# Kernel tuning notes

Hardware: AMD Instinct MI355X
Metric: run time of the kernel (lower is better)

The kernel has to match this reference:

```python
import jax, jax.numpy as jnp
import numpy as np

N_NODES = 100000
N_EDGES = 1600000
IN_FEAT = 128
HIDDEN = 64
N_CLASSES = 16


def setup_inputs() -> dict:
    key = jax.random.key(0)
    ks = jax.random.split(key, 8)
    x = jax.random.normal(ks[0], (N_NODES, IN_FEAT), dtype=jnp.float32)
    edge_index = jax.random.randint(ks[1], (2, N_EDGES), 0, N_NODES, dtype=jnp.int64)
    W1 = jax.random.normal(ks[2], (IN_FEAT, HIDDEN), dtype=jnp.float32) / np.sqrt(IN_FEAT)
    b1 = jnp.zeros((HIDDEN,), dtype=jnp.float32)
    W2 = jax.random.normal(ks[3], (HIDDEN, HIDDEN), dtype=jnp.float32) / np.sqrt(HIDDEN)
    b2 = jnp.zeros((HIDDEN,), dtype=jnp.float32)
    Wl = jax.random.normal(ks[4], (HIDDEN, N_CLASSES), dtype=jnp.float32) / np.sqrt(HIDDEN)
    bl = jnp.zeros((N_CLASSES,), dtype=jnp.float32)
    return {"x": x, "edge_index": edge_index, "W1": W1, "b1": b1,
            "W2": W2, "b2": b2, "Wl": Wl, "bl": bl}


def _gcn_norm(edge_index, n_nodes, dtype):
    # PyG GCNConv default: add self-loops, symmetric normalization
    # A_hat = D^{-1/2} (A + I) D^{-1/2}, degree computed at destination (col).
    loop = jnp.arange(n_nodes, dtype=edge_index.dtype)
    src = jnp.concatenate([edge_index[0], loop])
    dst = jnp.concatenate([edge_index[1], loop])
    deg = jax.ops.segment_sum(jnp.ones_like(dst, dtype=dtype), dst, num_segments=n_nodes)
    dinv = jnp.where(deg > 0, jax.lax.rsqrt(deg), 0.0).astype(dtype)
    norm = dinv[src] * dinv[dst]  # [E + N]
    return src, dst, norm


def _gcn_conv(h, src, dst, norm, W, b, n_nodes):
    hw = h @ W                                  # [N, out] linear first (GCNConv order)
    msg = hw[src] * norm[:, None]               # gather + edge-normalize, [E+N, out]
    out = jax.ops.segment_sum(msg, dst, num_segments=n_nodes)  # scatter-add
    return out + b


def reference(x, edge_index, W1, b1, W2, b2, Wl, bl):
    n = x.shape[0]
    src, dst, norm = _gcn_norm(edge_index, n, x.dtype)
    h = jax.nn.relu(_gcn_conv(x, src, dst, norm, W1, b1, n))
    h = jax.nn.relu(_gcn_conv(h, src, dst, norm, W2, b2, n))
    return h @ Wl + bl  # [N, num_classes] logits
```

## Files before the change

kernel.cpp:

```cpp
#include <hip/hip_runtime.h>
#include <hip/hip_fp16.h>
#include <math.h>

#define N_NODES 100000
#define N_EDGES 1600000
#define IN_FEAT 128
#define HIDDEN 64
#define N_CLASSES 16

#define TM 64
#define GBLK ((N_NODES + TM - 1) / TM)

#define NBUK 196
#define CB 4096
#define NCB ((N_EDGES + CB - 1) / CB)
#define NHB 128


__global__ void zero_buk_k(int* __restrict__ buk_cnt) {
    if (threadIdx.x < NBUK + 4) buk_cnt[threadIdx.x] = 0;
}

__global__ __launch_bounds__(256) void bukhist_k(const int* __restrict__ dst,
                                                 int* __restrict__ buk_cnt) {
    __shared__ int hist[NBUK + 4];
    int tid = threadIdx.x;
    if (tid < NBUK) hist[tid] = 0;
    __syncthreads();
    const int n4 = N_EDGES >> 2;
    for (int i4 = blockIdx.x * 256 + tid; i4 < n4; i4 += NHB * 256) {
        int4 d4 = ((const int4*)dst)[i4];
        atomicAdd(&hist[d4.x >> 9], 1);
        atomicAdd(&hist[d4.y >> 9], 1);
        atomicAdd(&hist[d4.z >> 9], 1);
        atomicAdd(&hist[d4.w >> 9], 1);
    }
    __syncthreads();
    if (tid < NBUK && hist[tid] != 0) atomicAdd(&buk_cnt[tid], hist[tid]);
}

__global__ __launch_bounds__(256) void buk_scan_k(const int* __restrict__ buk_cnt,
                                                  int* __restrict__ buk_off,
                                                  int* __restrict__ bcur) {
    __shared__ int sm[256];
    int t = threadIdx.x;
    int v = (t < NBUK) ? buk_cnt[t] : 0;
    sm[t] = v;
    __syncthreads();
    for (int s = 1; s < 256; s <<= 1) {
        int add = (t >= s) ? sm[t - s] : 0;
        __syncthreads();
        sm[t] += add;
        __syncthreads();
    }
    if (t < NBUK) {
        int excl = sm[t] - v;
        buk_off[t] = excl;
        bcur[t] = excl;
    }
    if (t == 0) buk_off[NBUK] = N_EDGES;
}


__global__ __launch_bounds__(256) void coarse_k(const int* __restrict__ src,
                                                const int* __restrict__ dst,
                                                int* __restrict__ bcur,
                                                int2* __restrict__ pairs) {
    __shared__ int hist[NBUK + 4], loff[NBUK + 4], cur[NBUK + 4], gbase[NBUK + 4];
    __shared__ int sc[256];
    __shared__ int2 stage[CB];
    int tid = threadIdx.x;
    int eb = blockIdx.x * CB;
    int nvalid = N_EDGES - eb;
    if (nvalid > CB) nvalid = CB;

    if (tid < NBUK) hist[tid] = 0;
    __syncthreads();

    int4 s4[4], d4[4];
    #pragma unroll
    for (int q = 0; q < 4; ++q) {
        int e4 = (eb >> 2) + tid + q * 256;
        if (e4 * 4 < N_EDGES) {
            s4[q] = ((const int4*)src)[e4];
            d4[q] = ((const int4*)dst)[e4];
        } else {
            d4[q] = make_int4(-1, -1, -1, -1);
            s4[q] = make_int4(0, 0, 0, 0);
        }
    }
    #pragma unroll
    for (int q = 0; q < 4; ++q) {
        if (d4[q].x >= 0) {
            atomicAdd(&hist[d4[q].x >> 9], 1);
            atomicAdd(&hist[d4[q].y >> 9], 1);
            atomicAdd(&hist[d4[q].z >> 9], 1);
            atomicAdd(&hist[d4[q].w >> 9], 1);
        }
    }
    __syncthreads();

    int v = (tid < NBUK) ? hist[tid] : 0;
    sc[tid] = v;
    __syncthreads();
    for (int s = 1; s < 256; s <<= 1) {
        int add = (tid >= s) ? sc[tid - s] : 0;
        __syncthreads();
        sc[tid] += add;
        __syncthreads();
    }
    if (tid < NBUK) {
        int excl = sc[tid] - v;
        loff[tid] = excl;
        cur[tid] = excl;
        gbase[tid] = atomicAdd(&bcur[tid], v);
    }
    __syncthreads();

    #pragma unroll
    for (int q = 0; q < 4; ++q) {
        if (d4[q].x >= 0) {
            int b, r;
            b = d4[q].x >> 9; r = atomicAdd(&cur[b], 1); stage[r] = make_int2(s4[q].x, d4[q].x);
            b = d4[q].y >> 9; r = atomicAdd(&cur[b], 1); stage[r] = make_int2(s4[q].y, d4[q].y);
            b = d4[q].z >> 9; r = atomicAdd(&cur[b], 1); stage[r] = make_int2(s4[q].z, d4[q].z);
            b = d4[q].w >> 9; r = atomicAdd(&cur[b], 1); stage[r] = make_int2(s4[q].w, d4[q].w);
        }
    }
    __syncthreads();

    for (int i = tid; i < nvalid; i += 256) {
        int2 p = stage[i];
        int b = p.y >> 9;
        pairs[gbase[b] + (i - loff[b])] = p;
    }
}


__global__ __launch_bounds__(256) void fine2_k(const int2* __restrict__ pairs,
                                               const int* __restrict__ buk_off,
                                               int* __restrict__ csr_src,
                                               int* __restrict__ row_ptr,
                                               float* __restrict__ dinv) {
    __shared__ int cnt[512];
    __shared__ int psc[256];
    __shared__ int cur[512];
    int b = blockIdx.x;
    int node0 = b * 512;
    int nn = N_NODES - node0;
    if (nn > 512) nn = 512;
    int tid = threadIdx.x;

    cnt[tid] = 0; cnt[tid + 256] = 0;
    __syncthreads();

    int e0 = buk_off[b];
    int e1 = buk_off[b + 1];

    for (int e = e0 + tid; e < e1; e += 256)
        atomicAdd(&cnt[pairs[e].y - node0], 1);
    __syncthreads();

    int c0 = cnt[2 * tid], c1 = cnt[2 * tid + 1];
    int p = c0 + c1;
    psc[tid] = p;
    __syncthreads();
    for (int s = 1; s < 256; s <<= 1) {
        int add = (tid >= s) ? psc[tid - s] : 0;
        __syncthreads();
        psc[tid] += add;
        __syncthreads();
    }
    int excl = psc[tid] - p;
    int g0 = e0 + excl;
    int g1 = g0 + c0;
    cur[2 * tid] = g0;
    cur[2 * tid + 1] = g1;
    if (2 * tid < nn) {
        row_ptr[node0 + 2 * tid] = g0;
        dinv[node0 + 2 * tid] = 1.0f / sqrtf((float)(c0 + 1));
    }
    if (2 * tid + 1 < nn) {
        row_ptr[node0 + 2 * tid + 1] = g1;
        dinv[node0 + 2 * tid + 1] = 1.0f / sqrtf((float)(c1 + 1));
    }
    if (b == NBUK - 1 && tid == 0) row_ptr[N_NODES] = N_EDGES;
    __syncthreads();

    for (int e = e0 + tid; e < e1; e += 256) {
        int2 pr = pairs[e];
        int pos = atomicAdd(&cur[pr.y - node0], 1);
        csr_src[pos] = pr.x;
    }
}


__global__ __launch_bounds__(256) void gemm1_tiled_k(const float* __restrict__ x,
                                                     const float* __restrict__ W,
                                                     const float* __restrict__ dinv,
                                                     __half* __restrict__ hws_h) {
    __shared__ float Ws[64][64];
    __shared__ float xt[64][68];
    int tid = threadIdx.x;
    int row0 = blockIdx.x * TM;
    int rgrp4 = (tid >> 4) * 4;
    int cgrp4 = (tid & 15) * 4;

    float acc[4][4];
    #pragma unroll
    for (int r = 0; r < 4; ++r)
        #pragma unroll
        for (int c = 0; c < 4; ++c) acc[r][c] = 0.0f;

    for (int k0 = 0; k0 < IN_FEAT; k0 += 64) {
        #pragma unroll
        for (int i = 0; i < 4; ++i) {
            int f4 = tid + i * 256;
            int kk = f4 >> 4, c4 = (f4 & 15) * 4;
            *(float4*)&Ws[kk][c4] = *(const float4*)&W[(size_t)(k0 + kk) * HIDDEN + c4];
        }
        #pragma unroll
        for (int i = 0; i < 4; ++i) {
            int f4 = tid + i * 256;
            int rr = f4 >> 4, kq = (f4 & 15) * 4;
            int row = row0 + rr;
            if (row >= N_NODES) row = N_NODES - 1;
            float4 v = *(const float4*)&x[(size_t)row * IN_FEAT + k0 + kq];
            xt[kq + 0][rr] = v.x; xt[kq + 1][rr] = v.y;
            xt[kq + 2][rr] = v.z; xt[kq + 3][rr] = v.w;
        }
        __syncthreads();

        #pragma unroll 16
        for (int kk = 0; kk < 64; ++kk) {
            float4 a = *(const float4*)&xt[kk][rgrp4];
            float4 b = *(const float4*)&Ws[kk][cgrp4];
            acc[0][0] += a.x * b.x; acc[0][1] += a.x * b.y; acc[0][2] += a.x * b.z; acc[0][3] += a.x * b.w;
            acc[1][0] += a.y * b.x; acc[1][1] += a.y * b.y; acc[1][2] += a.y * b.z; acc[1][3] += a.y * b.w;
            acc[2][0] += a.z * b.x; acc[2][1] += a.z * b.y; acc[2][2] += a.z * b.z; acc[2][3] += a.z * b.w;
            acc[3][0] += a.w * b.x; acc[3][1] += a.w * b.y; acc[3][2] += a.w * b.z; acc[3][3] += a.w * b.w;
        }
        __syncthreads();
    }

    #pragma unroll
    for (int r = 0; r < 4; ++r) {
        int row = row0 + rgrp4 + r;
        if (row < N_NODES) {
            float dn = dinv[row];
            __half2* ph = (__half2*)&hws_h[(size_t)row * HIDDEN + cgrp4];
            ph[0] = __floats2half2_rn(acc[r][0] * dn, acc[r][1] * dn);
            ph[1] = __floats2half2_rn(acc[r][2] * dn, acc[r][3] * dn);
        }
    }
}


__global__ __launch_bounds__(256) void gemm2_tiled_k(const float* __restrict__ agg,
                                                     const float* __restrict__ W,
                                                     const float* __restrict__ dinv,
                                                     __half* __restrict__ hws_h) {
    __shared__ float Ws[64][64];
    __shared__ float xt[64][68];
    int tid = threadIdx.x;
    int row0 = blockIdx.x * TM;
    int rgrp4 = (tid >> 4) * 4;
    int cgrp4 = (tid & 15) * 4;

    #pragma unroll
    for (int i = 0; i < 4; ++i) {
        int f4 = tid + i * 256;
        int kk = f4 >> 4, c4 = (f4 & 15) * 4;
        *(float4*)&Ws[kk][c4] = *(const float4*)&W[(size_t)kk * HIDDEN + c4];
    }
    #pragma unroll
    for (int i = 0; i < 4; ++i) {
        int f4 = tid + i * 256;
        int rr = f4 >> 4, kq = (f4 & 15) * 4;
        int row = row0 + rr;
        if (row >= N_NODES) row = N_NODES - 1;
        float4 v = *(const float4*)&agg[(size_t)row * HIDDEN + kq];
        xt[kq + 0][rr] = fmaxf(v.x, 0.f); xt[kq + 1][rr] = fmaxf(v.y, 0.f);
        xt[kq + 2][rr] = fmaxf(v.z, 0.f); xt[kq + 3][rr] = fmaxf(v.w, 0.f);
    }
    __syncthreads();

    float acc[4][4];
    #pragma unroll
    for (int r = 0; r < 4; ++r)
        #pragma unroll
        for (int c = 0; c < 4; ++c) acc[r][c] = 0.0f;

    #pragma unroll 16
    for (int kk = 0; kk < 64; ++kk) {
        float4 a = *(const float4*)&xt[kk][rgrp4];
        float4 b = *(const float4*)&Ws[kk][cgrp4];
        acc[0][0] += a.x * b.x; acc[0][1] += a.x * b.y; acc[0][2] += a.x * b.z; acc[0][3] += a.x * b.w;
        acc[1][0] += a.y * b.x; acc[1][1] += a.y * b.y; acc[1][2] += a.y * b.z; acc[1][3] += a.y * b.w;
        acc[2][0] += a.z * b.x; acc[2][1] += a.z * b.y; acc[2][2] += a.z * b.z; acc[2][3] += a.z * b.w;
        acc[3][0] += a.w * b.x; acc[3][1] += a.w * b.y; acc[3][2] += a.w * b.z; acc[3][3] += a.w * b.w;
    }

    #pragma unroll
    for (int r = 0; r < 4; ++r) {
        int row = row0 + rgrp4 + r;
        if (row < N_NODES) {
            float dn = dinv[row];
            __half2* ph = (__half2*)&hws_h[(size_t)row * HIDDEN + cgrp4];
            ph[0] = __floats2half2_rn(acc[r][0] * dn, acc[r][1] * dn);
            ph[1] = __floats2half2_rn(acc[r][2] * dn, acc[r][3] * dn);
        }
    }
}


__global__ __launch_bounds__(256) void pull_k(const int* __restrict__ row_ptr,
                                              const int* __restrict__ csr_src,
                                              const float* __restrict__ dinv,
                                              const __half* __restrict__ hws_h,
                                              const float* __restrict__ b,
                                              float* __restrict__ agg) {
    int node = __builtin_amdgcn_readfirstlane((blockIdx.x * 256 + threadIdx.x) >> 6);
    int lane = threadIdx.x & 63;
    if (node >= N_NODES) return;

    int start = __builtin_amdgcn_readfirstlane(row_ptr[node]);
    int end   = __builtin_amdgcn_readfirstlane(row_ptr[node + 1]);

    const __half* __restrict__ selfrow = hws_h + ((size_t)node << 6);
    float blane = b[lane];
    float a0 = __half2float(selfrow[lane]);
    float dn = dinv[node];

    float a1 = 0.f, a2 = 0.f, a3 = 0.f, a4 = 0.f, a5 = 0.f, a6 = 0.f, a7 = 0.f;

    int base = start;
    while (base < end) {
        int rem = end - base;
        int ci = base + lane;
        int lastci = end - 1;
        if (ci > lastci) ci = lastci;
        int idxv = csr_src[ci];
        int nch = rem < 64 ? rem : 64;

        for (int j = 0; j < nch; j += 16) {
            #pragma unroll
            for (int k = 0; k < 16; ++k) {
                int jj = j + k;
                int s = __builtin_amdgcn_readlane(idxv, jj);
                const __half* __restrict__ row = hws_h + ((size_t)s << 6);
                float w = (jj < rem) ? 1.f : 0.f;
                float v = __half2float(row[lane]);
                if (k == 0)      a0 += w * v;
                else if (k == 1) a1 += w * v;
                else if (k == 2) a2 += w * v;
                else if (k == 3) a3 += w * v;
                else if (k == 4) a4 += w * v;
                else if (k == 5) a5 += w * v;
                else if (k == 6) a6 += w * v;
                else if (k == 7) a7 += w * v;
                else if (k == 8)  a0 += w * v;
                else if (k == 9)  a1 += w * v;
                else if (k == 10) a2 += w * v;
                else if (k == 11) a3 += w * v;
                else if (k == 12) a4 += w * v;
                else if (k == 13) a5 += w * v;
                else if (k == 14) a6 += w * v;
                else              a7 += w * v;
            }
        }
        base += 64;
    }

    float sum = ((a0 + a1) + (a2 + a3)) + ((a4 + a5) + (a6 + a7));
    float* __restrict__ outrow = agg + ((size_t)node << 6);
    outrow[lane] = blane + dn * sum;
}


__global__ __launch_bounds__(256) void final_k(const float* __restrict__ agg,
                                               const float* __restrict__ Wl,
                                               const float* __restrict__ bl,
                                               float* __restrict__ out) {
    __shared__ float Ws[HIDDEN * N_CLASSES];
    __shared__ float hs[16][HIDDEN + 1];
    int tid = threadIdx.x;

    if (tid < HIDDEN * N_CLASSES / 4) ((float4*)Ws)[tid] = ((const float4*)Wl)[tid];

    int row0 = blockIdx.x * 16;
    for (int i = tid; i < 16 * HIDDEN; i += 256) {
        int rr = i >> 6;
        int kk = i & 63;
        hs[rr][kk] = fmaxf(agg[(size_t)(row0 + rr) * HIDDEN + kk], 0.0f);
    }
    __syncthreads();

    int col = tid & 15;
    int r = tid >> 4;
    float acc = bl[col];
    #pragma unroll
    for (int k = 0; k < HIDDEN; ++k)
        acc += hs[r][k] * Ws[k * N_CLASSES + col];
    out[(size_t)(row0 + r) * N_CLASSES + col] = acc;
}


extern "C" void kernel_launch(void* const* d_in, const int* in_sizes, int n_in,
                              void* d_out, int out_size, void* d_ws, size_t ws_size,
                              hipStream_t stream) {
    const float* x  = (const float*)d_in[0];
    const int*   ei = (const int*)d_in[1];
    const float* W1 = (const float*)d_in[2];
    const float* b1 = (const float*)d_in[3];
    const float* W2 = (const float*)d_in[4];
    const float* b2 = (const float*)d_in[5];
    const float* Wl = (const float*)d_in[6];
    const float* bl = (const float*)d_in[7];
    float* out = (float*)d_out;

    const int* src = ei;
    const int* dst = ei + N_EDGES;

    __half* hws_h  = (__half*)d_ws;
    float* agg     = (float*)(hws_h + (size_t)N_NODES * HIDDEN);
    int2*  pairs   = (int2*)agg;
    int*   csr_src = (int*)(agg + (size_t)N_NODES * HIDDEN);
    float* dinv    = (float*)(csr_src + N_EDGES);
    int*   row_ptr = (int*)(dinv + N_NODES);
    int*   buk_cnt = row_ptr + N_NODES + 4;
    int*   buk_off = buk_cnt + 200;
    int*   bcur    = buk_off + 200;

    zero_buk_k<<<1, 256, 0, stream>>>(buk_cnt);
    bukhist_k<<<NHB, 256, 0, stream>>>(dst, buk_cnt);
    buk_scan_k<<<1, 256, 0, stream>>>(buk_cnt, buk_off, bcur);
    coarse_k<<<NCB, 256, 0, stream>>>(src, dst, bcur, pairs);
    fine2_k<<<NBUK, 256, 0, stream>>>(pairs, buk_off, csr_src, row_ptr, dinv);

    gemm1_tiled_k<<<GBLK, 256, 0, stream>>>(x, W1, dinv, hws_h);
    pull_k<<<(N_NODES * 64 + 255) / 256, 256, 0, stream>>>(row_ptr, csr_src, dinv,
                                                           hws_h, b1, agg);

    gemm2_tiled_k<<<GBLK, 256, 0, stream>>>(agg, W2, dinv, hws_h);
    pull_k<<<(N_NODES * 64 + 255) / 256, 256, 0, stream>>>(row_ptr, csr_src, dinv,
                                                           hws_h, b2, agg);

    final_k<<<N_NODES / 16, 256, 0, stream>>>(agg, Wl, bl, out);
}
```

Measured before the change: 289.7 us.

## Replace coarse bucket sort with per-block count/scan/place and restructure pull gather

```diff
diff --git a/kernel.cpp b/kernel.cpp
--- a/kernel.cpp
+++ b/kernel.cpp
@@ -14,125 +14,88 @@
 #define NBUK 196
 #define CB 4096
 #define NCB ((N_EDGES + CB - 1) / CB)
-#define NHB 128
-
-
-__global__ void zero_buk_k(int* __restrict__ buk_cnt) {
-    if (threadIdx.x < NBUK + 4) buk_cnt[threadIdx.x] = 0;
-}
-
-__global__ __launch_bounds__(256) void bukhist_k(const int* __restrict__ dst,
-                                                 int* __restrict__ buk_cnt) {
+
+
+__global__ __launch_bounds__(256) void count_k(const int* __restrict__ dst,
+                                               int* __restrict__ blk_cnt) {
     __shared__ int hist[NBUK + 4];
     int tid = threadIdx.x;
     if (tid < NBUK) hist[tid] = 0;
     __syncthreads();
-    const int n4 = N_EDGES >> 2;
-    for (int i4 = blockIdx.x * 256 + tid; i4 < n4; i4 += NHB * 256) {
-        int4 d4 = ((const int4*)dst)[i4];
-        atomicAdd(&hist[d4.x >> 9], 1);
-        atomicAdd(&hist[d4.y >> 9], 1);
-        atomicAdd(&hist[d4.z >> 9], 1);
-        atomicAdd(&hist[d4.w >> 9], 1);
-    }
-    __syncthreads();
-    if (tid < NBUK && hist[tid] != 0) atomicAdd(&buk_cnt[tid], hist[tid]);
-}
-
-__global__ __launch_bounds__(256) void buk_scan_k(const int* __restrict__ buk_cnt,
-                                                  int* __restrict__ buk_off,
-                                                  int* __restrict__ bcur) {
-    __shared__ int sm[256];
-    int t = threadIdx.x;
-    int v = (t < NBUK) ? buk_cnt[t] : 0;
-    sm[t] = v;
-    __syncthreads();
-    for (int s = 1; s < 256; s <<= 1) {
-        int add = (t >= s) ? sm[t - s] : 0;
-        __syncthreads();
-        sm[t] += add;
-        __syncthreads();
-    }
-    if (t < NBUK) {
-        int excl = sm[t] - v;
-        buk_off[t] = excl;
-        bcur[t] = excl;
-    }
-    if (t == 0) buk_off[NBUK] = N_EDGES;
-}
-
-
-__global__ __launch_bounds__(256) void coarse_k(const int* __restrict__ src,
-                                                const int* __restrict__ dst,
-                                                int* __restrict__ bcur,
-                                                int2* __restrict__ pairs) {
-    __shared__ int hist[NBUK + 4], loff[NBUK + 4], cur[NBUK + 4], gbase[NBUK + 4];
-    __shared__ int sc[256];
-    __shared__ int2 stage[CB];
-    int tid = threadIdx.x;
     int eb = blockIdx.x * CB;
-    int nvalid = N_EDGES - eb;
-    if (nvalid > CB) nvalid = CB;
-
-    if (tid < NBUK) hist[tid] = 0;
-    __syncthreads();
-
-    int4 s4[4], d4[4];
     #pragma unroll
     for (int q = 0; q < 4; ++q) {
         int e4 = (eb >> 2) + tid + q * 256;
         if (e4 * 4 < N_EDGES) {
-            s4[q] = ((const int4*)src)[e4];
-            d4[q] = ((const int4*)dst)[e4];
-        } else {
-            d4[q] = make_int4(-1, -1, -1, -1);
-            s4[q] = make_int4(0, 0, 0, 0);
-        }
-    }
+            int4 d4 = ((const int4*)dst)[e4];
+            atomicAdd(&hist[d4.x >> 9], 1);
+            atomicAdd(&hist[d4.y >> 9], 1);
+            atomicAdd(&hist[d4.z >> 9], 1);
+            atomicAdd(&hist[d4.w >> 9], 1);
+        }
+    }
+    __syncthreads();
+    if (tid < NBUK) blk_cnt[blockIdx.x * NBUK + tid] = hist[tid];
+}
+
+__global__ __launch_bounds__(512) void colscan_k(int* __restrict__ blk_cnt,
+                                                 int* __restrict__ coltot) {
+    __shared__ int sm[512];
+    int b = blockIdx.x;
+    int t = threadIdx.x;
+    int v = (t < NCB) ? blk_cnt[t * NBUK + b] : 0;
+    sm[t] = v;
+    __syncthreads();
+    for (int s = 1; s < 512; s <<= 1) {
+        int add = (t >= s) ? sm[t - s] : 0;
+        __syncthreads();
+        sm[t] += add;
+        __syncthreads();
+    }
+    if (t < NCB) blk_cnt[t * NBUK + b] = sm[t] - v;
+    if (t == NCB - 1) coltot[b] = sm[t];
+}
+
+__global__ __launch_bounds__(256) void bukoff_k(const int* __restrict__ coltot,
+                                                int* __restrict__ buk_off) {
+    __shared__ int sm[256];
+    int t = threadIdx.x;
+    int v = (t < NBUK) ? coltot[t] : 0;
+    sm[t] = v;
+    __syncthreads();
+    for (int s = 1; s < 256; s <<= 1) {
+        int add = (t >= s) ? sm[t - s] : 0;
+        __syncthreads();
+        sm[t] += add;
+        __syncthreads();
+    }
+    if (t < NBUK) buk_off[t] = sm[t] - v;
+    if (t == 0) buk_off[NBUK] = N_EDGES;
+}
+
+__global__ __launch_bounds__(256) void place_k(const int* __restrict__ src,
+                                               const int* __restrict__ dst,
+                                               const int* __restrict__ colpre,
+                                               const int* __restrict__ buk_off,
+                                               int2* __restrict__ pairs) {
+    __shared__ int cur[NBUK + 4];
+    int tid = threadIdx.x;
+    int blk = blockIdx.x;
+    if (tid < NBUK) cur[tid] = buk_off[tid] + colpre[blk * NBUK + tid];
+    __syncthreads();
+    int eb = blk * CB;
     #pragma unroll
     for (int q = 0; q < 4; ++q) {
-        if (d4[q].x >= 0) {
-            atomicAdd(&hist[d4[q].x >> 9], 1);
-            atomicAdd(&hist[d4[q].y >> 9], 1);
-            atomicAdd(&hist[d4[q].z >> 9], 1);
-            atomicAdd(&hist[d4[q].w >> 9], 1);
-        }
-    }
-    __syncthreads();
-
-    int v = (tid < NBUK) ? hist[tid] : 0;
-    sc[tid] = v;
-    __syncthreads();
-    for (int s = 1; s < 256; s <<= 1) {
-        int add = (tid >= s) ? sc[tid - s] : 0;
-        __syncthreads();
-        sc[tid] += add;
-        __syncthreads();
-    }
-    if (tid < NBUK) {
-        int excl = sc[tid] - v;
-        loff[tid] = excl;
-        cur[tid] = excl;
-        gbase[tid] = atomicAdd(&bcur[tid], v);
-    }
-    __syncthreads();
-
-    #pragma unroll
-    for (int q = 0; q < 4; ++q) {
-        if (d4[q].x >= 0) {
-            int b, r;
-            b = d4[q].x >> 9; r = atomicAdd(&cur[b], 1); stage[r] = make_int2(s4[q].x, d4[q].x);
-            b = d4[q].y >> 9; r = atomicAdd(&cur[b], 1); stage[r] = make_int2(s4[q].y, d4[q].y);
-            b = d4[q].z >> 9; r = atomicAdd(&cur[b], 1); stage[r] = make_int2(s4[q].z, d4[q].z);
-            b = d4[q].w >> 9; r = atomicAdd(&cur[b], 1); stage[r] = make_int2(s4[q].w, d4[q].w);
-        }
-    }
-    __syncthreads();
-
-    for (int i = tid; i < nvalid; i += 256) {
-        int2 p = stage[i];
-        int b = p.y >> 9;
-        pairs[gbase[b] + (i - loff[b])] = p;
+        int e4 = (eb >> 2) + tid + q * 256;
+        if (e4 * 4 < N_EDGES) {
+            int4 s4 = ((const int4*)src)[e4];
+            int4 d4 = ((const int4*)dst)[e4];
+            int r;
+            r = atomicAdd(&cur[d4.x >> 9], 1); pairs[r] = make_int2(s4.x, d4.x);
+            r = atomicAdd(&cur[d4.y >> 9], 1); pairs[r] = make_int2(s4.y, d4.y);
+            r = atomicAdd(&cur[d4.z >> 9], 1); pairs[r] = make_int2(s4.z, d4.z);
+            r = atomicAdd(&cur[d4.w >> 9], 1); pairs[r] = make_int2(s4.w, d4.w);
+        }
     }
 }
 
@@ -314,6 +277,16 @@
 }
 
 
+#define GATH(K, ACC)                                                        \
+    { int s_ = __builtin_amdgcn_readlane(idxv, (C) + (K));                  \
+      const __half* row_ = hws_h + ((size_t)s_ << 6);                       \
+      float w_ = ((K) < rem) ? 1.f : 0.f;                                   \
+      ACC += w_ * __half2float(row_[lane]); }
+
+#define GATH8(B)                                                            \
+    GATH((B) + 0, a0) GATH((B) + 1, a1) GATH((B) + 2, a2) GATH((B) + 3, a3) \
+    GATH((B) + 4, a4) GATH((B) + 5, a5) GATH((B) + 6, a6) GATH((B) + 7, a7)
+
 __global__ __launch_bounds__(256) void pull_k(const int* __restrict__ row_ptr,
                                               const int* __restrict__ csr_src,
                                               const float* __restrict__ dinv,
@@ -336,38 +309,20 @@
 
     int base = start;
     while (base < end) {
+        int ci = base + lane;
+        int last = end - 1;
+        if (ci > last) ci = last;
+        int idxv = csr_src[ci];
+
         int rem = end - base;
-        int ci = base + lane;
-        int lastci = end - 1;
-        if (ci > lastci) ci = lastci;
-        int idxv = csr_src[ci];
-        int nch = rem < 64 ? rem : 64;
-
-        for (int j = 0; j < nch; j += 16) {
-            #pragma unroll
-            for (int k = 0; k < 16; ++k) {
-                int jj = j + k;
-                int s = __builtin_amdgcn_readlane(idxv, jj);
-                const __half* __restrict__ row = hws_h + ((size_t)s << 6);
-                float w = (jj < rem) ? 1.f : 0.f;
-                float v = __half2float(row[lane]);
-                if (k == 0)      a0 += w * v;
-                else if (k == 1) a1 += w * v;
-                else if (k == 2) a2 += w * v;
-                else if (k == 3) a3 += w * v;
-                else if (k == 4) a4 += w * v;
-                else if (k == 5) a5 += w * v;
-                else if (k == 6) a6 += w * v;
-                else if (k == 7) a7 += w * v;
-                else if (k == 8)  a0 += w * v;
-                else if (k == 9)  a1 += w * v;
-                else if (k == 10) a2 += w * v;
-                else if (k == 11) a3 += w * v;
-                else if (k == 12) a4 += w * v;
-                else if (k == 13) a5 += w * v;
-                else if (k == 14) a6 += w * v;
-                else              a7 += w * v;
-            }
+        {
+            const int C = 0;
+            GATH8(0) GATH8(8) GATH8(16) GATH8(24)
+        }
+        if (base + 32 < end) {
+            const int C = 32;
+            rem = end - base - 32;
+            GATH8(0) GATH8(8) GATH8(16) GATH8(24)
         }
         base += 64;
     }
@@ -430,12 +385,13 @@
     int*   row_ptr = (int*)(dinv + N_NODES);
     int*   buk_cnt = row_ptr + N_NODES + 4;
     int*   buk_off = buk_cnt + 200;
-    int*   bcur    = buk_off + 200;
-
-    zero_buk_k<<<1, 256, 0, stream>>>(buk_cnt);
-    bukhist_k<<<NHB, 256, 0, stream>>>(dst, buk_cnt);
-    buk_scan_k<<<1, 256, 0, stream>>>(buk_cnt, buk_off, bcur);
-    coarse_k<<<NCB, 256, 0, stream>>>(src, dst, bcur, pairs);
+    int*   coltot  = buk_off + 200;
+    int*   blk_cnt = csr_src;
+
+    count_k<<<NCB, 256, 0, stream>>>(dst, blk_cnt);
+    colscan_k<<<NBUK, 512, 0, stream>>>(blk_cnt, coltot);
+    bukoff_k<<<1, 256, 0, stream>>>(coltot, buk_off);
+    place_k<<<NCB, 256, 0, stream>>>(src, dst, blk_cnt, buk_off, pairs);
     fine2_k<<<NBUK, 256, 0, stream>>>(pairs, buk_off, csr_src, row_ptr, dinv);
 
     gemm1_tiled_k<<<GBLK, 256, 0, stream>>>(x, W1, dinv, hws_h);
```

Measured after the change: 288.3 us. No clear change (-0.5%).
